# Kernel tuning notes

Measured on AMD Instinct MI355X. Metric: run time of the kernel, lower is better.

The kernel has to match this reference:

```python
import jax, jax.numpy as jnp
import numpy as np

BS = 320        # batch_size (per-view)
D = 128         # projection feature dim
SIGMA = 0.07    # rbf gamma = 1/sigma
C_BOX = 1.0     # box constraint on alpha
REG = 0.1       # diagonal regularizer


def setup_inputs() -> dict:
    key = jax.random.key(0)
    z = jax.random.normal(key, (2 * BS, D), dtype=jnp.float32)
    return {"z": z}


def reference(z):
    bs = z.shape[0] // 2
    nn_ = bs - 1
    dtype = z.dtype

    # L2-normalize features
    z = z / jnp.linalg.norm(z, axis=1, keepdims=True)

    gamma = 1.0 / float(SIGMA)
    K = jnp.exp(-gamma * (2.0 - 2.0 * (z[:bs] @ z.T)))        # (bs, 2bs)

    # ---- QP assembly (no-grad in original) ----
    KK = jax.lax.stop_gradient(K[:, :bs])                      # (bs, bs)
    eye = jnp.eye(bs, dtype=dtype)
    KK_d0 = KK * (1.0 - eye)
    # Delta[t,i,j] = 1 + reg*eye[i,j] + KK[i,j] - KK_d0[t,i] - KK_d0[t,j]
    Delta = (1.0 + REG * eye + KK)[None, :, :] \
            - KK_d0[:, None, :] - KK_d0[:, :, None]            # (bs, bs, bs)

    # For each t, drop row t and column t -> (bs, nn, nn)
    t_idx = jnp.arange(bs)
    j = jnp.arange(nn_)
    idx = j[None, :] + (j[None, :] >= t_idx[:, None]).astype(j.dtype)  # (bs, nn)
    DD = Delta[t_idx[:, None, None], idx[:, :, None], idx[:, None, :]]

    # Batched linear solve: DD alpha = 2*1
    rhs = 2.0 * jnp.ones((bs, nn_, 1), dtype=dtype)
    alpha_y = jnp.linalg.solve(DD, rhs)[..., 0]                # (bs, nn)
    alpha_y = jax.lax.stop_gradient(
        jnp.clip(jax.nn.relu(alpha_y), 0.0, C_BOX))
    alpha_x = alpha_y.sum(1)                                   # (bs,)

    # ---- loss terms (grad flows through K here) ----
    Ks = K[:, bs:]                                             # (bs, bs)
    # Kn = Ks^T with diagonal removed row-wise, then transposed -> (nn, bs)
    Kn = Ks.T[t_idx[:, None], idx].T

    pos_terms = jnp.diagonal(Ks)                               # (Ks * pos_mask).sum(1)
    pos_loss = (alpha_x * pos_terms).mean()
    neg_loss = (alpha_y.T * Kn).sum() / bs
    loss = neg_loss - pos_loss

    num_zero = (alpha_y == 0).sum().astype(dtype) / alpha_y.size
    sparsity = (alpha_y == C_BOX).sum().astype(dtype) / \
               ((alpha_y > 0).sum().astype(dtype) + 1e-10)

    return (loss, pos_terms.mean(), Kn.mean(), sparsity, num_zero, 0.0)
```

## Files before the change

### kernel.cpp

```cpp
#include <hip/hip_runtime.h>
#include <math.h>

#define BSZ 320
#define N2  640
#define DIM 128
#define GAM (1.0/0.07)

__device__ __forceinline__ double wave_red(double v) {
    #pragma unroll
    for (int off = 32; off > 0; off >>= 1) v += __shfl_down(v, off, 64);
    return v;
}

__launch_bounds__(128)
__global__ void k_prep(const float* __restrict__ z, float* __restrict__ zn,
                       int* __restrict__ counter) {
    const int row = blockIdx.x, k = threadIdx.x;
    if (row == 0 && k == 0) *counter = 0;
    double v = (double)z[row * DIM + k];
    __shared__ double s2[2];
    double w = wave_red(v * v);
    int wave = k >> 6, lane = k & 63;
    if (lane == 0) s2[wave] = w;
    __syncthreads();
    zn[row * DIM + k] = (float)(v / sqrt(s2[0] + s2[1]));
}

__launch_bounds__(320)
__global__ void k_gram(const float* __restrict__ zn, double* __restrict__ E,
                       double* __restrict__ KnT, double* __restrict__ rE,
                       double* __restrict__ ssq) {
    const int tid = threadIdx.x;
    const int i0  = blockIdx.x * 2;
    const int jh  = blockIdx.y;
    __shared__ float  zc[320][36];
    __shared__ float  zi[2][128];
    __shared__ double sE[2][5], sQ[2][5];

    if (tid < 256) {
        int r = tid >> 7, k = tid & 127;
        zi[r][k] = zn[(i0 + r) * DIM + k];
    }

    float cr0 = 0.f, cr1 = 0.f;
    for (int kc = 0; kc < 4; kc++) {
        const int k0 = kc * 32;
        __syncthreads();
        #pragma unroll
        for (int it = 0; it < 8; it++) {
            int f = it * 320 + tid;
            int row = f >> 3, c4 = f & 7;
            *(float4*)&zc[row][c4 * 4] =
                *(const float4*)(zn + (jh * 320 + row) * DIM + k0 + c4 * 4);
        }
        __syncthreads();
        #pragma unroll
        for (int k4 = 0; k4 < 8; k4++) {
            float4 b  = *(const float4*)&zc[tid][k4 * 4];
            float4 a0 = *(const float4*)&zi[0][k0 + k4 * 4];
            float4 a1 = *(const float4*)&zi[1][k0 + k4 * 4];
            cr0 = fmaf(a0.x, b.x, cr0); cr1 = fmaf(a1.x, b.x, cr1);
            cr0 = fmaf(a0.y, b.y, cr0); cr1 = fmaf(a1.y, b.y, cr1);
            cr0 = fmaf(a0.z, b.z, cr0); cr1 = fmaf(a1.z, b.z, cr1);
            cr0 = fmaf(a0.w, b.w, cr0); cr1 = fmaf(a1.w, b.w, cr1);
        }
    }
    double v0 = exp(-GAM * (2.0 - 2.0 * (double)cr0));
    double v1 = exp(-GAM * (2.0 - 2.0 * (double)cr1));
    const int wave = tid >> 6, lane = tid & 63;
    if (jh == 0) {
        double e0 = (tid == i0    ) ? 0.0 : v0;
        double e1 = (tid == i0 + 1) ? 0.0 : v1;
        E[(i0    ) * BSZ + tid] = e0;
        E[(i0 + 1) * BSZ + tid] = e1;
        double q0 = e0 * e0, q1 = e1 * e1;
        e0 = wave_red(e0); q0 = wave_red(q0);
        e1 = wave_red(e1); q1 = wave_red(q1);
        if (lane == 0) { sE[0][wave] = e0; sQ[0][wave] = q0;
                         sE[1][wave] = e1; sQ[1][wave] = q1; }
        __syncthreads();
        if (tid < 2) {
            double se = 0.0, sq = 0.0;
            for (int w = 0; w < 5; w++) { se += sE[tid][w]; sq += sQ[tid][w]; }
            rE[i0 + tid] = se; ssq[i0 + tid] = sq;
        }
    } else {
        KnT[tid * BSZ + i0]     = v0;
        KnT[tid * BSZ + i0 + 1] = v1;
    }
}

__launch_bounds__(320)
__global__ void k_cf(const double* __restrict__ E, const double* __restrict__ KnT,
                     const double* __restrict__ rE, const double* __restrict__ ssq,
                     double* __restrict__ partials, int* __restrict__ counter,
                     float* __restrict__ out) {
    const int t = blockIdx.x, tid = threadIdx.x;
    const int wave = tid >> 6, lane = tid & 63;
    __shared__ double sred[5][7];
    __shared__ double sc[8];
    __shared__ int lastflag;
    const double a = 1.0 / 1.1, c = 1.0 / 321.1;
    const double q = 1.0 - 320.0 * c;

    double rEi  = rE[tid];
    double Ereg = E[t * BSZ + tid];
    double kn   = KnT[t * BSZ + tid];
    if (tid == t) sc[6] = kn;

    {
        double s1 = wave_red(rEi);
        double s2 = wave_red(Ereg * rEi);
        if (lane == 0) { sred[wave][0] = s1; sred[wave][1] = s2; }
    }
    __syncthreads();
    if (tid == 0) {
        double S = 0, mv = 0;
        for (int w = 0; w < 5; w++) { S += sred[w][0]; mv += sred[w][1]; }
        double rEt = rE[t], ssqt = ssq[t];
        double pt  = a * q - a * a * q * (rEt - c * S);
        double b   = 320.0 * a * q - a * a * q * q * S;
        double up  = a * q * rEt - a * a * q * (mv - c * S * rEt);
        double sc1 = a * ssqt - a * c * rEt * rEt;
        double Wtt = -a * c * rEt;
        double Mtt = a * (1.0 - c) - a * a * (c * c * S - 2.0 * c * rEt);
        double s11 = 1.0 - up, s12 = -b, s21 = -sc1, s22 = 1.0 - up;
        double det = s11 * s22 - s12 * s21;
        double r1 = 2.0 * b, r2 = 2.0 * up;
        double be1 = (s22 * r1 - s12 * r2) / det;
        double be2 = (s11 * r2 - s21 * r1) / det;
        double g1  = (s22 * pt - s12 * Wtt) / det;
        double g2  = (s11 * Wtt - s21 * pt) / det;
        double ytt = 2.0 * pt + be1 * Wtt + be2 * pt;
        double dt  = Mtt + g1 * Wtt + g2 * pt;
        double rho = ytt / dt;
        sc[0] = rEt;
        sc[1] = S;
        sc[2] = 2.0 + be2 - rho * g2;
        sc[3] = be1 - rho * g1;
        sc[4] = -rho;
    }
    __syncthreads();

    {
        double rEt = sc[0], S = sc[1], cP = sc[2], cW = sc[3], cM = sc[4];
        double s_neg = 0, s_al = 0, s_kn = 0, cz = 0, c1v = 0, cpos = 0;
        if (tid != t) {
            double p_i = a * q - a * a * q * (rEi - c * S);
            double V   = a * Ereg - a * c * rEt;
            double Mi  = -a * c - a * a * (Ereg - c * (rEt + rEi) + c * c * S);
            double x = cP * p_i + cW * V + cM * Mi;
            double alpha = fmin(fmax(x, 0.0), 1.0);
            s_neg = alpha * kn; s_al = alpha; s_kn = kn;
            cz   = (x <= 0.0) ? 1.0 : 0.0;
            c1v  = (x >= 1.0) ? 1.0 : 0.0;
            cpos = (x > 0.0) ? 1.0 : 0.0;
        }
        s_neg = wave_red(s_neg); s_al = wave_red(s_al); s_kn = wave_red(s_kn);
        cz = wave_red(cz); c1v = wave_red(c1v); cpos = wave_red(cpos);
        if (lane == 0) {
            sred[wave][0] = s_neg; sred[wave][1] = s_al; sred[wave][2] = s_kn;
            sred[wave][3] = cz;    sred[wave][4] = c1v;  sred[wave][5] = cpos;
        }
    }
    __syncthreads();
    if (tid == 0) {
        double a0 = 0, a1 = 0, a2 = 0, a3 = 0, a4 = 0, a5 = 0;
        for (int w = 0; w < 5; w++) {
            a0 += sred[w][0]; a1 += sred[w][1]; a2 += sred[w][2];
            a3 += sred[w][3]; a4 += sred[w][4]; a5 += sred[w][5];
        }
        partials[t * 8 + 0] = a0;
        partials[t * 8 + 1] = a1 * sc[6];
        partials[t * 8 + 2] = a2;
        partials[t * 8 + 3] = a3;
        partials[t * 8 + 4] = a4;
        partials[t * 8 + 5] = a5;
        partials[t * 8 + 6] = sc[6];
        __threadfence();
        int ticket = atomicAdd(counter, 1);
        lastflag = (ticket == BSZ - 1) ? 1 : 0;
    }
    __syncthreads();

    if (lastflag) {
        __threadfence();
        double v0 = partials[tid * 8 + 0], v1 = partials[tid * 8 + 1];
        double v2 = partials[tid * 8 + 2], v3 = partials[tid * 8 + 3];
        double v4 = partials[tid * 8 + 4], v5 = partials[tid * 8 + 5];
        double v6 = partials[tid * 8 + 6];
        v0 = wave_red(v0); v1 = wave_red(v1); v2 = wave_red(v2);
        v3 = wave_red(v3); v4 = wave_red(v4); v5 = wave_red(v5);
        v6 = wave_red(v6);
        if (lane == 0) {
            sred[wave][0] = v0; sred[wave][1] = v1; sred[wave][2] = v2;
            sred[wave][3] = v3; sred[wave][4] = v4; sred[wave][5] = v5;
            sred[wave][6] = v6;
        }
        __syncthreads();
        if (tid == 0) {
            double b0 = 0, b1 = 0, b2 = 0, b3 = 0, b4 = 0, b5 = 0, b6 = 0;
            for (int w = 0; w < 5; w++) {
                b0 += sred[w][0]; b1 += sred[w][1]; b2 += sred[w][2];
                b3 += sred[w][3]; b4 += sred[w][4]; b5 += sred[w][5];
                b6 += sred[w][6];
            }
            out[0] = (float)((b0 - b1) / 320.0);
            out[1] = (float)(b6 / 320.0);
            out[2] = (float)(b2 / (319.0 * 320.0));
            out[3] = (float)(b4 / (b5 + 1e-10));
            out[4] = (float)(b3 / (320.0 * 319.0));
            out[5] = 0.0f;
        }
    }
}

extern "C" void kernel_launch(void* const* d_in, const int* in_sizes, int n_in,
                              void* d_out, int out_size, void* d_ws, size_t ws_size,
                              hipStream_t stream) {
    const float* z = (const float*)d_in[0];
    float* out = (float*)d_out;
    double* ws = (double*)d_ws;

    double* E        = ws;
    double* KnT      = E + 102400;
    double* rE       = KnT + 102400;
    double* ssq      = rE + 320;
    double* partials = ssq + 320;
    int*    counter  = (int*)(partials + 320 * 8);
    float*  zn       = (float*)(counter + 16);

    k_prep<<<dim3(N2), dim3(DIM), 0, stream>>>(z, zn, counter);
    k_gram<<<dim3(BSZ / 2, 2), dim3(BSZ), 0, stream>>>(zn, E, KnT, rE, ssq);
    k_cf  <<<dim3(BSZ), dim3(BSZ), 0, stream>>>(E, KnT, rE, ssq, partials, counter, out);
}
```

Baseline: 31.28 us.

## Transpose raw z, fold normalization into gram, store kernel matrices as float

The prep kernel now only transposes raw z into a k-major float4 layout instead of normalizing rows. Normalization is folded into the gram kernel, which computes each column's squared norm alongside the dot products and rescales the cosine afterwards. The gram kernel runs one block per t computing both E and Kn rows with coalesced stores, replacing the strided KnT writes. E and Kn are now stored as float instead of double, halving intermediate traffic at some cost in precision for the downstream solve.

```diff
diff --git a/kernel.cpp b/kernel.cpp
--- a/kernel.cpp
+++ b/kernel.cpp
@@ -12,86 +12,83 @@
     return v;
 }
 
-__launch_bounds__(128)
-__global__ void k_prep(const float* __restrict__ z, float* __restrict__ zn,
-                       int* __restrict__ counter) {
-    const int row = blockIdx.x, k = threadIdx.x;
-    if (row == 0 && k == 0) *counter = 0;
-    double v = (double)z[row * DIM + k];
-    __shared__ double s2[2];
-    double w = wave_red(v * v);
-    int wave = k >> 6, lane = k & 63;
-    if (lane == 0) s2[wave] = w;
-    __syncthreads();
-    zn[row * DIM + k] = (float)(v / sqrt(s2[0] + s2[1]));
+__launch_bounds__(256)
+__global__ void k_tr(const float* __restrict__ z, float* __restrict__ znT4,
+                     int* __restrict__ counter) {
+    const int tid = threadIdx.x;
+    const int row = blockIdx.x * 2 + (tid >> 7);
+    const int k   = tid & 127;
+    if (blockIdx.x == 0 && tid == 0) *counter = 0;
+    znT4[(k >> 2) * (N2 * 4) + row * 4 + (k & 3)] = z[row * DIM + k];
 }
 
 __launch_bounds__(320)
-__global__ void k_gram(const float* __restrict__ zn, double* __restrict__ E,
-                       double* __restrict__ KnT, double* __restrict__ rE,
-                       double* __restrict__ ssq) {
-    const int tid = threadIdx.x;
-    const int i0  = blockIdx.x * 2;
-    const int jh  = blockIdx.y;
-    __shared__ float  zc[320][36];
-    __shared__ float  zi[2][128];
-    __shared__ double sE[2][5], sQ[2][5];
-
+__global__ void k_gram(const float* __restrict__ z, const float* __restrict__ znT4,
+                       float* __restrict__ E32, float* __restrict__ Kn32,
+                       double* __restrict__ rE, double* __restrict__ ssq) {
+    const int t = blockIdx.x, tid = threadIdx.x;
+    const int wave = tid >> 6, lane = tid & 63;
+    __shared__ float zA[DIM], zB[DIM];
+    __shared__ double s2[5];
+    __shared__ double snrm[2];
+    __shared__ double sred[5][2];
+
+    double w = 0.0;
     if (tid < 256) {
         int r = tid >> 7, k = tid & 127;
-        zi[r][k] = zn[(i0 + r) * DIM + k];
-    }
-
-    float cr0 = 0.f, cr1 = 0.f;
-    for (int kc = 0; kc < 4; kc++) {
-        const int k0 = kc * 32;
-        __syncthreads();
-        #pragma unroll
-        for (int it = 0; it < 8; it++) {
-            int f = it * 320 + tid;
-            int row = f >> 3, c4 = f & 7;
-            *(float4*)&zc[row][c4 * 4] =
-                *(const float4*)(zn + (jh * 320 + row) * DIM + k0 + c4 * 4);
-        }
-        __syncthreads();
-        #pragma unroll
-        for (int k4 = 0; k4 < 8; k4++) {
-            float4 b  = *(const float4*)&zc[tid][k4 * 4];
-            float4 a0 = *(const float4*)&zi[0][k0 + k4 * 4];
-            float4 a1 = *(const float4*)&zi[1][k0 + k4 * 4];
-            cr0 = fmaf(a0.x, b.x, cr0); cr1 = fmaf(a1.x, b.x, cr1);
-            cr0 = fmaf(a0.y, b.y, cr0); cr1 = fmaf(a1.y, b.y, cr1);
-            cr0 = fmaf(a0.z, b.z, cr0); cr1 = fmaf(a1.z, b.z, cr1);
-            cr0 = fmaf(a0.w, b.w, cr0); cr1 = fmaf(a1.w, b.w, cr1);
-        }
-    }
-    double v0 = exp(-GAM * (2.0 - 2.0 * (double)cr0));
-    double v1 = exp(-GAM * (2.0 - 2.0 * (double)cr1));
-    const int wave = tid >> 6, lane = tid & 63;
-    if (jh == 0) {
-        double e0 = (tid == i0    ) ? 0.0 : v0;
-        double e1 = (tid == i0 + 1) ? 0.0 : v1;
-        E[(i0    ) * BSZ + tid] = e0;
-        E[(i0 + 1) * BSZ + tid] = e1;
-        double q0 = e0 * e0, q1 = e1 * e1;
-        e0 = wave_red(e0); q0 = wave_red(q0);
-        e1 = wave_red(e1); q1 = wave_red(q1);
-        if (lane == 0) { sE[0][wave] = e0; sQ[0][wave] = q0;
-                         sE[1][wave] = e1; sQ[1][wave] = q1; }
-        __syncthreads();
-        if (tid < 2) {
-            double se = 0.0, sq = 0.0;
-            for (int w = 0; w < 5; w++) { se += sE[tid][w]; sq += sQ[tid][w]; }
-            rE[i0 + tid] = se; ssq[i0 + tid] = sq;
-        }
-    } else {
-        KnT[tid * BSZ + i0]     = v0;
-        KnT[tid * BSZ + i0 + 1] = v1;
+        float v = z[(r == 0 ? t : BSZ + t) * DIM + k];
+        if (r == 0) zA[k] = v; else zB[k] = v;
+        w = (double)v * (double)v;
+    }
+    w = wave_red(w);
+    if (lane == 0) s2[wave] = w;
+    __syncthreads();
+    if (tid == 0) {
+        snrm[0] = 1.0 / sqrt(s2[0] + s2[1]);
+        snrm[1] = 1.0 / sqrt(s2[2] + s2[3]);
+    }
+    __syncthreads();
+
+    const float4* znv = (const float4*)znT4;
+    const float4* zAv = (const float4*)zA;
+    const float4* zBv = (const float4*)zB;
+    float cA = 0.f, cB = 0.f;
+    double rr = 0.0;
+    #pragma unroll
+    for (int k4 = 0; k4 < 32; k4++) {
+        float4 v = znv[k4 * N2 + tid];
+        float4 a = zAv[k4];
+        float4 b = zBv[k4];
+        cA = fmaf(a.x, v.x, cA); cB = fmaf(b.x, v.x, cB);
+        rr = fma((double)v.x, (double)v.x, rr);
+        cA = fmaf(a.y, v.y, cA); cB = fmaf(b.y, v.y, cB);
+        rr = fma((double)v.y, (double)v.y, rr);
+        cA = fmaf(a.z, v.z, cA); cB = fmaf(b.z, v.z, cB);
+        rr = fma((double)v.z, (double)v.z, rr);
+        cA = fmaf(a.w, v.w, cA); cB = fmaf(b.w, v.w, cB);
+        rr = fma((double)v.w, (double)v.w, rr);
+    }
+    double sI = 1.0 / sqrt(rr);
+    double cosA = (double)cA * snrm[0] * sI;
+    double cosB = (double)cB * snrm[1] * sI;
+    double Et = (tid == t) ? 0.0 : exp(-GAM * (2.0 - 2.0 * cosA));
+    double kn = exp(-GAM * (2.0 - 2.0 * cosB));
+    E32[t * BSZ + tid]  = (float)Et;
+    Kn32[t * BSZ + tid] = (float)kn;
+
+    double se = wave_red(Et);
+    double sq = wave_red(Et * Et);
+    if (lane == 0) { sred[wave][0] = se; sred[wave][1] = sq; }
+    __syncthreads();
+    if (tid == 0) {
+        double a0 = 0.0, a1 = 0.0;
+        for (int ww = 0; ww < 5; ww++) { a0 += sred[ww][0]; a1 += sred[ww][1]; }
+        rE[t] = a0; ssq[t] = a1;
     }
 }
 
 __launch_bounds__(320)
-__global__ void k_cf(const double* __restrict__ E, const double* __restrict__ KnT,
+__global__ void k_cf(const float* __restrict__ E32, const float* __restrict__ Kn32,
                      const double* __restrict__ rE, const double* __restrict__ ssq,
                      double* __restrict__ partials, int* __restrict__ counter,
                      float* __restrict__ out) {
@@ -104,8 +101,8 @@
     const double q = 1.0 - 320.0 * c;
 
     double rEi  = rE[tid];
-    double Ereg = E[t * BSZ + tid];
-    double kn   = KnT[t * BSZ + tid];
+    double Ereg = (double)E32[t * BSZ + tid];
+    double kn   = (double)Kn32[t * BSZ + tid];
     if (tid == t) sc[6] = kn;
 
     {
@@ -220,17 +217,17 @@
                               hipStream_t stream) {
     const float* z = (const float*)d_in[0];
     float* out = (float*)d_out;
-    double* ws = (double*)d_ws;
-
-    double* E        = ws;
-    double* KnT      = E + 102400;
-    double* rE       = KnT + 102400;
-    double* ssq      = rE + 320;
-    double* partials = ssq + 320;
-    int*    counter  = (int*)(partials + 320 * 8);
-    float*  zn       = (float*)(counter + 16);
-
-    k_prep<<<dim3(N2), dim3(DIM), 0, stream>>>(z, zn, counter);
-    k_gram<<<dim3(BSZ / 2, 2), dim3(BSZ), 0, stream>>>(zn, E, KnT, rE, ssq);
-    k_cf  <<<dim3(BSZ), dim3(BSZ), 0, stream>>>(E, KnT, rE, ssq, partials, counter, out);
-}
+    char* ws = (char*)d_ws;
+
+    float*  znT4     = (float*)(ws);
+    float*  E32      = (float*)(ws + 327680);
+    float*  Kn32     = (float*)(ws + 737280);
+    double* rE       = (double*)(ws + 1146880);
+    double* ssq      = (double*)(ws + 1149440);
+    double* partials = (double*)(ws + 1152000);
+    int*    counter  = (int*)(ws + 1172480);
+
+    k_tr  <<<dim3(BSZ), dim3(256), 0, stream>>>(z, znT4, counter);
+    k_gram<<<dim3(BSZ), dim3(BSZ), 0, stream>>>(z, znT4, E32, Kn32, rE, ssq);
+    k_cf  <<<dim3(BSZ), dim3(BSZ), 0, stream>>>(E32, Kn32, rE, ssq, partials, counter, out);
+}
```

Measured after the change: 56.16 us. 1.8x slower.
